# Kernel tuning notes

Hardware: AMD Instinct MI355X
Metric: run time of the kernel (lower is better)

The kernel has to match this reference:

```python
import jax, jax.numpy as jnp
import numpy as np

B, C_IN, T, H, W = 4, 512, 4, 56, 56
G, GP, K = 8, 64, 56            # groups, group_planes, kernel_size (H == K)
OUT = G * GP                     # out_channels = 512
EPS = 1e-5


def setup_inputs() -> dict:
    key = jax.random.key(0)
    ks = jax.random.split(key, 9)
    x = jax.random.normal(ks[0], (B, C_IN, T, H, W), jnp.float32)
    w_qkv = jax.random.normal(ks[1], (2 * OUT, C_IN), jnp.float32) * np.sqrt(1.0 / C_IN)
    g_qkv = jax.random.uniform(ks[2], (2 * OUT,), jnp.float32, 0.5, 1.5)
    b_qkv = jax.random.normal(ks[3], (2 * OUT,), jnp.float32) * 0.1
    relative = jax.random.normal(ks[4], (2 * GP, 2 * K - 1), jnp.float32) * np.sqrt(1.0 / GP)
    g_sim = jax.random.uniform(ks[5], (3 * G,), jnp.float32, 0.5, 1.5)
    b_sim = jax.random.normal(ks[6], (3 * G,), jnp.float32) * 0.1
    g_out = jax.random.uniform(ks[7], (2 * OUT,), jnp.float32, 0.5, 1.5)
    b_out = jax.random.normal(ks[8], (2 * OUT,), jnp.float32) * 0.1
    return {"x": x, "w_qkv": w_qkv, "g_qkv": g_qkv, "b_qkv": b_qkv,
            "relative": relative, "g_sim": g_sim, "b_sim": b_sim,
            "g_out": g_out, "b_out": b_out}


def _bn(x, gamma, beta, axes):
    # training-mode batchnorm: batch stats over `axes`, per channel (dim 1)
    mean = jnp.mean(x, axes, keepdims=True)
    var = jnp.var(x, axes, keepdims=True)
    shp = [1] * x.ndim
    shp[1] = -1
    return gamma.reshape(shp) * (x - mean) * jax.lax.rsqrt(var + EPS) + beta.reshape(shp)


def reference(x, w_qkv, g_qkv, b_qkv, relative, g_sim, b_sim, g_out, b_out):
    # axial='height': (B,C,T,H,W) -> (B,T,W,C,H), attend along H
    xp = jnp.transpose(x, (0, 2, 4, 1, 3)).reshape(B * T * W, C_IN, H)
    # 1x1 Conv1d + BatchNorm1d
    qkv = _bn(jnp.einsum('oc,nch->noh', w_qkv, xp), g_qkv, b_qkv, (0, 2))
    qkv = qkv.reshape(-1, G, 2 * GP, H)
    q, k, v = qkv[:, :, :GP // 2], qkv[:, :, GP // 2:GP], qkv[:, :, GP:]
    qk = jnp.einsum('bgci,bgcj->bgij', q, k)
    # relative position embeddings gathered per (i, j) offset
    idx = jnp.arange(K)[:, None] - jnp.arange(K)[None, :] + K - 1  # (K, K)
    emb = relative[:, idx]                                         # (2*GP, K, K)
    q_e, k_e, v_e = emb[:GP // 2], emb[GP // 2:GP], emb[GP:]
    qr = jnp.einsum('bgci,cij->bgij', q, q_e)
    kr = jnp.swapaxes(jnp.einsum('bgci,cij->bgij', k, k_e), 2, 3)
    sim = _bn(jnp.concatenate([qk, qr, kr], axis=1), g_sim, b_sim, (0, 2, 3))
    sim = sim.reshape(-1, 3, G, H, H).sum(axis=1)
    sim = jax.nn.softmax(sim, axis=3)
    sv = jnp.einsum('bgij,bgcj->bgci', sim, v)
    sve = jnp.einsum('bgij,cij->bgci', sim, v_e)
    out = jnp.concatenate([sv, sve], axis=-1).reshape(-1, 2 * OUT, H)
    out = _bn(out, g_out, b_out, (0, 2))
    out = out.reshape(B, T, W, OUT, 2, H).sum(axis=-2)
    return jnp.transpose(out, (0, 3, 1, 4, 2))  # (B, OUT, T, H, W)
```

## Files before the change

kernel.cpp:

```cpp
#include <hip/hip_runtime.h>
#include <hip/hip_bf16.h>

#define EPS 1e-5f
typedef __hip_bfloat16 bf;
typedef __attribute__((ext_vector_type(8))) short bf16x8;
typedef __attribute__((ext_vector_type(4))) short s16x4;
typedef __attribute__((ext_vector_type(4))) float f32x4;

#define MFMA16(a, b, c) __builtin_amdgcn_mfma_f32_16x16x32_bf16(a, b, c, 0, 0, 0)

#define WS_QSUM     0
#define WS_QSQ      4096
#define WS_SIMSUM   8192
#define WS_SIMSQ    9728
#define WS_OUTSUM   11264
#define WS_OUTSQ    19456
#define WS_ZERO_END 27648
#define WS_AQKV     27648
#define WS_BQKV     28672
#define WS_ASIM     29696
#define WS_BSIM     29728
#define WS_AOUT     29760
#define WS_BOUT     30784

__device__ __forceinline__ void gload_lds16(const void* g, void* l) {
    __builtin_amdgcn_global_load_lds(
        (const __attribute__((address_space(1))) void*)g,
        (__attribute__((address_space(3))) void*)l, 16, 0, 0);
}
__device__ __forceinline__ float bfbits2f(short b) {
    return __uint_as_float(((uint32_t)(unsigned short)b) << 16);
}
__device__ __forceinline__ short f2bfbits(float f) {
    return (short)__hip_bfloat16_raw(__float2bfloat16(f)).x;
}

__global__ __launch_bounds__(256) void k0_transpose(const float* __restrict__ x,
                                                    bf* __restrict__ xbt) {
    int bid = blockIdx.x;
    int h = bid % 56, bt = bid / 56;
    int b = bt >> 2, t = bt & 3;
    __shared__ short tile[512 * 57];
    const float* src = x + (((size_t)(b * 512) * 4 + t) * 3136) + h * 56;
    for (int e = threadIdx.x; e < 512 * 56; e += 256) {
        int c = e / 56, w = e - c * 56;
        tile[c * 57 + w] = f2bfbits(src[(size_t)c * 12544 + w]);
    }
    __syncthreads();
    short* dst = reinterpret_cast<short*>(xbt);
    size_t pbase = ((size_t)bt * 56) * 56 + h;
    for (int e = threadIdx.x; e < 512 * 56; e += 256) {
        int w = e >> 9, c = e & 511;
        dst[(pbase + (size_t)w * 56) * 512 + c] = tile[c * 57 + w];
    }
}

__global__ __launch_bounds__(256) void kw_conv(const float* __restrict__ w, bf* __restrict__ wb) {
    int i = (blockIdx.x * 256 + threadIdx.x) * 4;
#pragma unroll
    for (int u = 0; u < 4; ++u) wb[i + u] = __float2bfloat16(w[i + u]);
}

__global__ __launch_bounds__(256) void kprep(const float* __restrict__ rel,
                                             short* __restrict__ relTq,
                                             short* __restrict__ relTk,
                                             short* __restrict__ relBv) {
    int tid = blockIdx.x * 256 + threadIdx.x;
    if (tid < 3584) {
        int d = tid >> 5, c = tid & 31;
        relTq[tid] = f2bfbits(d < 111 ? rel[c * 111 + d] : 0.f);
        relTk[tid] = f2bfbits(d < 111 ? rel[(32 + c) * 111 + d] : 0.f);
    } else if (tid < 11776) {
        int u = tid - 3584, c = u >> 7, d = u & 127;
        relBv[u] = f2bfbits(d < 111 ? rel[(64 + c) * 111 + d] : 0.f);
    }
}

__global__ __launch_bounds__(256) void k1_mfma(const bf* __restrict__ xbt,
                                               const bf* __restrict__ wb,
                                               short* __restrict__ qkP,
                                               short* __restrict__ vP,
                                               float* __restrict__ qsum,
                                               float* __restrict__ qsq) {
    __shared__ __align__(16) short As[8192];
    __shared__ __align__(16) short Bs[7168];
    int tid = threadIdx.x;
    int g  = blockIdx.x;
    int p0 = blockIdx.y * 112;
    int o0 = g * 128;
    const short* aG = reinterpret_cast<const short*>(wb);
    const short* bG = reinterpret_cast<const short*>(xbt);
    int wv = tid >> 6, l = tid & 63, r16 = l & 15, q4 = l >> 4;

    f32x4 acc[2][7];
#pragma unroll
    for (int i = 0; i < 2; ++i)
#pragma unroll
        for (int j = 0; j < 7; ++j) acc[i][j] = (f32x4){0.f, 0.f, 0.f, 0.f};

    int rowa0 = wv * 32 + r16, rowa1 = rowa0 + 16;

    for (int k0 = 0; k0 < 512; k0 += 64) {
        int ch = tid;
#pragma unroll
        for (int it = 0; it < 4; ++it, ch += 256) {
            int row = ch >> 3, c = ch & 7;
            int gc = (c ^ row) & 7;
            gload_lds16(aG + (((size_t)(o0 + row)) << 9) + k0 + gc * 8, &As[ch << 3]);
        }
        ch = tid;
#pragma unroll
        for (int it = 0; it < 3; ++it, ch += 256) {
            int row = ch >> 3, c = ch & 7;
            int gc = (c ^ row) & 7;
            gload_lds16(bG + (((size_t)(p0 + row)) << 9) + k0 + gc * 8, &Bs[ch << 3]);
        }
        if (tid < 128) {
            int u = tid + 768;
            int row = u >> 3, c = u & 7;
            int gc = (c ^ row) & 7;
            gload_lds16(bG + (((size_t)(p0 + row)) << 9) + k0 + gc * 8, &Bs[u << 3]);
        }
        __syncthreads();
#pragma unroll
        for (int kk = 0; kk < 2; ++kk) {
            int wch = kk * 4 + q4;
            bf16x8 a0 = *reinterpret_cast<const bf16x8*>(&As[rowa0 * 64 + ((wch ^ rowa0) & 7) * 8]);
            bf16x8 a1 = *reinterpret_cast<const bf16x8*>(&As[rowa1 * 64 + ((wch ^ rowa1) & 7) * 8]);
#pragma unroll
            for (int j = 0; j < 7; ++j) {
                int rowb = j * 16 + r16;
                bf16x8 bj = *reinterpret_cast<const bf16x8*>(&Bs[rowb * 64 + ((wch ^ rowb) & 7) * 8]);
                acc[0][j] = MFMA16(a0, bj, acc[0][j]);
                acc[1][j] = MFMA16(a1, bj, acc[1][j]);
            }
        }
        __syncthreads();
    }
    int bkt = blockIdx.y & 3;
#pragma unroll
    for (int i = 0; i < 2; ++i)
#pragma unroll
        for (int r = 0; r < 4; ++r) {
            float sA = 0.f, sB = 0.f;
#pragma unroll
            for (int j = 0; j < 7; ++j) { float v = acc[i][j][r]; sA += v; sB += v * v; }
#pragma unroll
            for (int mk = 1; mk < 16; mk <<= 1) { sA += __shfl_xor(sA, mk); sB += __shfl_xor(sB, mk); }
            if (r16 == 0) {
                int o = o0 + wv * 32 + i * 16 + q4 * 4 + r;
                atomicAdd(&qsum[o * 4 + bkt], sA);
                atomicAdd(&qsq [o * 4 + bkt], sB);
            }
        }
#pragma unroll
    for (int j = 0; j < 7; ++j) {
        int p = p0 + j * 16 + r16;
        size_t rowb = ((size_t)g * 50176 + p) * 64;
#pragma unroll
        for (int i = 0; i < 2; ++i) {
            int op = wv * 32 + i * 16 + q4 * 4;
            s16x4 pk;
#pragma unroll
            for (int r = 0; r < 4; ++r) pk[r] = f2bfbits(acc[i][j][r]);
            short* dst = (op < 64) ? (qkP + rowb + op) : (vP + rowb + (op - 64));
            *reinterpret_cast<s16x4*>(dst) = pk;
        }
    }
}

__global__ __launch_bounds__(256) void k1b_coef(const float* __restrict__ qsum, const float* __restrict__ qsq,
                                                const float* __restrict__ gamma, const float* __restrict__ beta,
                                                float* __restrict__ a_c, float* __restrict__ b_c) {
    int o = blockIdx.x * 256 + threadIdx.x;
    float s = qsum[o * 4] + qsum[o * 4 + 1] + qsum[o * 4 + 2] + qsum[o * 4 + 3];
    float s2 = qsq[o * 4] + qsq[o * 4 + 1] + qsq[o * 4 + 2] + qsq[o * 4 + 3];
    float inv = 1.f / 50176.f;
    float mean = s * inv;
    float var = s2 * inv - mean * mean;
    float a = gamma[o] * rsqrtf(var + EPS);
    a_c[o] = a; b_c[o] = beta[o] - a * mean;
}

__global__ __launch_bounds__(512) void kbn2(const short* __restrict__ qkP,
                                            short* __restrict__ vP,
                                            const float* __restrict__ aq, const float* __restrict__ bq,
                                            const short* __restrict__ relTq,
                                            const short* __restrict__ relTk,
                                            float* __restrict__ ssum, float* __restrict__ ssq) {
    __shared__ __align__(16) short qkTl[5120];
    __shared__ short vtl[64 * 57];
    __shared__ float red[48];
    int blk = blockIdx.x, n = blk >> 3, g = blk & 7, tid = threadIdx.x;
    size_t sb = ((size_t)g * 50176 + (size_t)n * 56) * 64;
    const short* qsrc = qkP + sb;
    short* vsrc = vP + sb;
    for (int u = tid; u < 448; u += 512) {
        int i = u >> 3, c0 = (u & 7) << 3;
        bf16x8 raw = *reinterpret_cast<const bf16x8*>(qsrc + i * 64 + c0);
        bf16x8 t;
#pragma unroll
        for (int uu = 0; uu < 8; ++uu) {
            int o = g * 128 + c0 + uu;
            t[uu] = f2bfbits(aq[o] * bfbits2f(raw[uu]) + bq[o]);
        }
        *reinterpret_cast<bf16x8*>(&qkTl[((c0 & 32) ? 2560 : 0) + i * 40 + (c0 & 31)]) = t;
    }
    for (int u = tid; u < 640; u += 512) {
        int part = u / 320, r = u - part * 320;
        qkTl[part * 2560 + (56 + r / 40) * 40 + (r % 40)] = 0;
    }
    for (int u = tid; u < 448; u += 512) {
        int i = u >> 3, c0 = (u & 7) << 3;
        bf16x8 raw = *reinterpret_cast<const bf16x8*>(vsrc + i * 64 + c0);
#pragma unroll
        for (int uu = 0; uu < 8; ++uu) {
            int o = g * 128 + 64 + c0 + uu;
            vtl[(c0 + uu) * 57 + i] = f2bfbits(aq[o] * bfbits2f(raw[uu]) + bq[o]);
        }
    }
    __syncthreads();
    for (int u = tid; u < 448; u += 512) {
        int c = u / 7, h0 = (u - c * 7) * 8;
        bf16x8 t;
#pragma unroll
        for (int uu = 0; uu < 8; ++uu) t[uu] = vtl[c * 57 + h0 + uu];
        *reinterpret_cast<bf16x8*>(vsrc + c * 56 + h0) = t;
    }
    int w = tid >> 6, l = tid & 63, m = w >> 1, s = w & 1, la = l & 15, lb = l >> 4;
    bf16x8 aqf = *reinterpret_cast<const bf16x8*>(&qkTl[(m * 16 + la) * 40 + lb * 8]);
    bf16x8 akf = *reinterpret_cast<const bf16x8*>(&qkTl[2560 + (m * 16 + la) * 40 + lb * 8]);
    float s0 = 0, s1 = 0, s2v = 0, q0 = 0, q1 = 0, q2 = 0;
#pragma unroll
    for (int t = 0; t < 2; ++t) {
        int nt = 2 * s + t;
        bf16x8 bk = *reinterpret_cast<const bf16x8*>(&qkTl[2560 + (nt * 16 + la) * 40 + lb * 8]);
        f32x4 acc = {0, 0, 0, 0};
        acc = MFMA16(aqf, bk, acc);
        int j = nt * 16 + la;
        if (j < 56) {
#pragma unroll
            for (int r = 0; r < 4; ++r) {
                int i = m * 16 + lb * 4 + r;
                if (i < 56) { float v = acc[r]; s0 += v; q0 += v * v; }
            }
        }
    }
    int ndt = s ? 3 : 4, dt0 = s * 4;
    for (int t = 0; t < ndt; ++t) {
        int dt = dt0 + t;
        bf16x8 br = *reinterpret_cast<const bf16x8*>(relTq + (dt * 16 + la) * 32 + lb * 8);
        f32x4 acc = {0, 0, 0, 0};
        acc = MFMA16(aqf, br, acc);
        int d = dt * 16 + la;
#pragma unroll
        for (int r = 0; r < 4; ++r) {
            int i = m * 16 + lb * 4 + r;
            if (i < 56 && d >= i && d <= i + 55) { float v = acc[r]; s1 += v; q1 += v * v; }
        }
    }
    for (int t = 0; t < ndt; ++t) {
        int dt = dt0 + t;
        bf16x8 br = *reinterpret_cast<const bf16x8*>(relTk + (dt * 16 + la) * 32 + lb * 8);
        f32x4 acc = {0, 0, 0, 0};
        acc = MFMA16(akf, br, acc);
        int d = dt * 16 + la;
#pragma unroll
        for (int r = 0; r < 4; ++r) {
            int j = m * 16 + lb * 4 + r;
            if (j < 56 && d >= j && d <= j + 55) { float v = acc[r]; s2v += v; q2 += v * v; }
        }
    }
    float vals[6] = {s0, s1, s2v, q0, q1, q2};
#pragma unroll
    for (int v = 0; v < 6; ++v) {
        for (int off = 32; off; off >>= 1) vals[v] += __shfl_down(vals[v], off);
        if (l == 0) red[v * 8 + w] = vals[v];
    }
    __syncthreads();
    if (tid < 6) {
        float tot = 0;
#pragma unroll
        for (int k = 0; k < 8; ++k) tot += red[tid * 8 + k];
        int comp = (tid < 3) ? tid : tid - 3;
        int ch = comp * 8 + g;
        int bkt = blk & 63;
        atomicAdd((tid < 3 ? ssum : ssq) + ch * 64 + bkt, tot);
    }
}

__global__ void k2b_coef(const float* __restrict__ ssum, const float* __restrict__ ssq,
                         const float* __restrict__ gs, const float* __restrict__ bs,
                         float* __restrict__ a_c, float* __restrict__ b_c) {
    int c = threadIdx.x;
    if (c >= 24) return;
    float s = 0, s2 = 0;
    for (int k = 0; k < 64; ++k) { s += ssum[c * 64 + k]; s2 += ssq[c * 64 + k]; }
    float inv = 1.f / 2809856.f;
    float mean = s * inv;
    float var = s2 * inv - mean * mean;
    float a = gs[c] * rsqrtf(var + EPS);
    a_c[c] = a; b_c[c] = bs[c] - a * mean;
}

__global__ __launch_bounds__(512, 6) void k3_mfma(const short* __restrict__ relTq,
                                                  const short* __restrict__ relTk,
                                                  const short* __restrict__ relBv,
                                                  short* __restrict__ qkP,
                                                  short* __restrict__ vP,
                                                  const float* __restrict__ aq, const float* __restrict__ bq,
                                                  const float* __restrict__ asim, const float* __restrict__ bsim,
                                                  float* __restrict__ osum, float* __restrict__ osq) {
    __shared__ __align__(16) char smem[51680];
    short* qkTl = (short*)smem;
    float* qkl  = (float*)(smem + 10240);
    short* Sql  = (short*)(smem + 23008);
    short* Krl  = (short*)(smem + 35776);
    short* simB = (short*)(smem + 23008);
    short* Pb   = (short*)(smem + 32224);
    short* vBl  = (short*)smem;
    float* red  = (float*)(smem + 49632);

    int blk = blockIdx.x, n = blk >> 3, g = blk & 7, tid = threadIdx.x;
    size_t sb = ((size_t)g * 50176 + (size_t)n * 56) * 64;
    short* svdst = qkP + sb;
    short* vHs   = vP + sb;
    for (int u = tid; u < 448; u += 512) {
        int i = u >> 3, c0 = (u & 7) << 3;
        bf16x8 raw = *reinterpret_cast<const bf16x8*>(svdst + i * 64 + c0);
        bf16x8 t;
#pragma unroll
        for (int uu = 0; uu < 8; ++uu) {
            int o = g * 128 + c0 + uu;
            t[uu] = f2bfbits(aq[o] * bfbits2f(raw[uu]) + bq[o]);
        }
        *reinterpret_cast<bf16x8*>(&qkTl[((c0 & 32) ? 2560 : 0) + i * 40 + (c0 & 31)]) = t;
    }
    for (int u = tid; u < 640; u += 512) {
        int part = u / 320, r = u - part * 320;
        qkTl[part * 2560 + (56 + r / 40) * 40 + (r % 40)] = 0;
    }
    __syncthreads();

    int w = tid >> 6, l = tid & 63, m = w >> 1, s = w & 1, la = l & 15, lb = l >> 4;
    {
        bf16x8 aqf = *reinterpret_cast<const bf16x8*>(&qkTl[(m * 16 + la) * 40 + lb * 8]);
        bf16x8 akf = *reinterpret_cast<const bf16x8*>(&qkTl[(64 + m * 16 + la) * 40 + lb * 8]);
#pragma unroll
        for (int t = 0; t < 2; ++t) {
            int nt = 2 * s + t;
            bf16x8 bk = *reinterpret_cast<const bf16x8*>(&qkTl[(64 + nt * 16 + la) * 40 + lb * 8]);
            f32x4 acc = {0, 0, 0, 0};
            acc = MFMA16(aqf, bk, acc);
            int j = nt * 16 + la;
            if (j < 56) {
#pragma unroll
                for (int r = 0; r < 4; ++r) {
                    int i = m * 16 + lb * 4 + r;
                    if (i < 56) qkl[i * 57 + j] = acc[r];
                }
            }
        }
        int ndt = s ? 3 : 4, dt0 = s * 4;
        for (int t = 0; t < ndt; ++t) {
            int dt = dt0 + t;
            bf16x8 br = *reinterpret_cast<const bf16x8*>(relTq + (dt * 16 + la) * 32 + lb * 8);
            f32x4 acc = {0, 0, 0, 0};
            acc = MFMA16(aqf, br, acc);
            int d = dt * 16 + la;
#pragma unroll
            for (int r = 0; r < 4; ++r) {
                int i = m * 16 + lb * 4 + r;
                if (i < 56) Sql[i * 114 + d] = f2bfbits(acc[r]);
            }
        }
        for (int t = 0; t < ndt; ++t) {
            int dt = dt0 + t;
            bf16x8 br = *reinterpret_cast<const bf16x8*>(relTk + (dt * 16 + la) * 32 + lb * 8);
            f32x4 acc = {0, 0, 0, 0};
            acc = MFMA16(akf, br, acc);
            int d = dt * 16 + la;
#pragma unroll
            for (int r = 0; r < 4; ++r) {
                int j = m * 16 + lb * 4 + r;
                if (j < 56) Krl[j * 114 + d] = f2bfbits(acc[r]);
            }
        }
    }
    __syncthreads();

    for (int u = tid; u < 448; u += 512) {
        int c = u / 7, ch = u - c * 7;
        bf16x8 raw = *reinterpret_cast<const bf16x8*>(vHs + c * 56 + ch * 8);
        *reinterpret_cast<bf16x8*>(&vBl[c * 72 + ch * 8]) = raw;
    }
    if (tid < 128) {
        int c = tid >> 1, chp = tid & 1;
        bf16x8 z = {0, 0, 0, 0, 0, 0, 0, 0};
        *reinterpret_cast<bf16x8*>(&vBl[c * 72 + 56 + chp * 8]) = z;
    }
    float a0 = asim[g], a1 = asim[8 + g], a2 = asim[16 + g];
    float bb = bsim[g] + bsim[8 + g] + bsim[16 + g];
    float p[7];
#pragma unroll
    for (int rr = 0; rr < 7; ++rr) {
        int i = w * 7 + rr;
        float sc = -1e30f;
        if (l < 56) {
            sc = a0 * qkl[i * 57 + l]
               + a1 * bfbits2f(Sql[i * 114 + (i - l + 55)])
               + a2 * bfbits2f(Krl[l * 114 + (l - i + 55)]) + bb;
        }
        float mx = sc;
#pragma unroll
        for (int off = 32; off; off >>= 1) mx = fmaxf(mx, __shfl_xor(mx, off));
        float e = (l < 56) ? __expf(sc - mx) : 0.f;
        float su = e;
#pragma unroll
        for (int off = 32; off; off >>= 1) su += __shfl_xor(su, off);
        p[rr] = e / su;
    }
    __syncthreads();

#pragma unroll
    for (int rr = 0; rr < 7; ++rr) {
        int i = w * 7 + rr;
        short pv = f2bfbits(p[rr]);
        simB[i * 72 + l] = (l < 56) ? pv : (short)0;
        if (l < 56) Pb[i * 136 + (i - l + 55)] = pv;
        if (l < i || l > i + 55) Pb[i * 136 + l] = 0;
        if (l > i - 9) Pb[i * 136 + l + 64] = 0;
        if (l < 8) Pb[i * 136 + l + 128] = 0;
    }
    __syncthreads();

    f32x4 sva[2]  = {{0, 0, 0, 0}, {0, 0, 0, 0}};
    f32x4 svea[2] = {{0, 0, 0, 0}, {0, 0, 0, 0}};
#pragma unroll
    for (int ks = 0; ks < 2; ++ks) {
        bf16x8 av = *reinterpret_cast<const bf16x8*>(&vBl[(m * 16 + la) * 72 + ks * 32 + lb * 8]);
#pragma unroll
        for (int t = 0; t < 2; ++t) {
            int nt = 2 * s + t;
            bf16x8 bsf = *reinterpret_cast<const bf16x8*>(&simB[(nt * 16 + la) * 72 + ks * 32 + lb * 8]);
            sva[t] = MFMA16(av, bsf, sva[t]);
        }
    }
#pragma unroll
    for (int ks = 0; ks < 4; ++ks) {
        bf16x8 ar = *reinterpret_cast<const bf16x8*>(relBv + (m * 16 + la) * 128 + ks * 32 + lb * 8);
#pragma unroll
        for (int t = 0; t < 2; ++t) {
            int nt = 2 * s + t;
            bf16x8 bp = *reinterpret_cast<const bf16x8*>(&Pb[(nt * 16 + la) * 136 + ks * 32 + lb * 8]);
            svea[t] = MFMA16(ar, bp, svea[t]);
        }
    }
    float st0[4] = {0, 0, 0, 0}, st1[4] = {0, 0, 0, 0}, st2[4] = {0, 0, 0, 0}, st3[4] = {0, 0, 0, 0};
#pragma unroll
    for (int t = 0; t < 2; ++t) {
        int i = (2 * s + t) * 16 + la;
        bool ok = i < 56;
#pragma unroll
        for (int r = 0; r < 4; ++r) {
            int c = m * 16 + lb * 4 + r;
            float va = sva[t][r], ve = svea[t][r];
            if (ok) {
                svdst[c * 56 + i] = f2bfbits(va);
                vHs  [c * 56 + i] = f2bfbits(ve);
                st0[r] += va; st1[r] += va * va; st2[r] += ve; st3[r] += ve * ve;
            }
        }
    }
#pragma unroll
    for (int r = 0; r < 4; ++r) {
#pragma unroll
        for (int mk = 1; mk < 16; mk <<= 1) {
            st0[r] += __shfl_xor(st0[r], mk);
            st1[r] += __shfl_xor(st1[r], mk);
            st2[r] += __shfl_xor(st2[r], mk);
            st3[r] += __shfl_xor(st3[r], mk);
        }
    }
    if (la == 0) {
#pragma unroll
        for (int r = 0; r < 4; ++r) {
            int c = m * 16 + lb * 4 + r;
            red[(0 * 64 + c) * 2 + s] = st0[r];
            red[(1 * 64 + c) * 2 + s] = st1[r];
            red[(2 * 64 + c) * 2 + s] = st2[r];
            red[(3 * 64 + c) * 2 + s] = st3[r];
        }
    }
    __syncthreads();
    if (tid < 64) {
        int c = tid, o2 = (g * 64 + c) * 2, bkt = blk & 7;
        atomicAdd(&osum[o2 * 8 + bkt],       red[(0 * 64 + c) * 2] + red[(0 * 64 + c) * 2 + 1]);
        atomicAdd(&osq [o2 * 8 + bkt],       red[(1 * 64 + c) * 2] + red[(1 * 64 + c) * 2 + 1]);
        atomicAdd(&osum[(o2 + 1) * 8 + bkt], red[(2 * 64 + c) * 2] + red[(2 * 64 + c) * 2 + 1]);
        atomicAdd(&osq [(o2 + 1) * 8 + bkt], red[(3 * 64 + c) * 2] + red[(3 * 64 + c) * 2 + 1]);
    }
}

__global__ __launch_bounds__(256) void k3b_coef(const float* __restrict__ osum, const float* __restrict__ osq,
                                                const float* __restrict__ go, const float* __restrict__ bo,
                                                float* __restrict__ a_c, float* __restrict__ b_c) {
    int o = blockIdx.x * 256 + threadIdx.x;
    float s = 0, s2 = 0;
#pragma unroll
    for (int k = 0; k < 8; ++k) { s += osum[o * 8 + k]; s2 += osq[o * 8 + k]; }
    float inv = 1.f / 50176.f;
    float mean = s * inv;
    float var = s2 * inv - mean * mean;
    float a = go[o] * rsqrtf(var + EPS);
    a_c[o] = a; b_c[o] = bo[o] - a * mean;
}

__global__ __launch_bounds__(256) void k4_out(const short* __restrict__ svq,
                                              const short* __restrict__ sve,
                                              const float* __restrict__ ao, const float* __restrict__ bo,
                                              float* __restrict__ out) {
    int blk = blockIdx.x;
    int oc = blk & 511, bt = blk >> 9;
    int b = bt >> 2, tt = bt & 3;
    int g = oc >> 6, c = oc & 63;
    __shared__ float tile[56][57];
    int tid = threadIdx.x;
    int o_sv = oc * 2, o_sve = oc * 2 + 1;
    float asv = ao[o_sv], bsv = bo[o_sv], asve = ao[o_sve], bsve = bo[o_sve];
    float badd = bsv + bsve;
    int nbase = (b * 4 + tt) * 56;
    for (int e = tid; e < 3136; e += 256) {
        int wq = e / 56, h = e - wq * 56;
        size_t idx = ((size_t)g * 50176 + (size_t)(nbase + wq) * 56) * 64 + c * 56 + h;
        tile[wq][h] = asv * bfbits2f(svq[idx]) + asve * bfbits2f(sve[idx]) + badd;
    }
    __syncthreads();
    size_t ob = ((size_t)(b * 512 + oc) * 4 + tt) * 3136;
    for (int e = tid; e < 3136; e += 256) {
        int h = e / 56, wq = e - h * 56;
        out[ob + h * 56 + wq] = tile[wq][h];
    }
}

extern "C" void kernel_launch(void* const* d_in, const int* in_sizes, int n_in,
                              void* d_out, int out_size, void* d_ws, size_t ws_size,
                              hipStream_t stream) {
    (void)in_sizes; (void)n_in; (void)out_size; (void)ws_size;
    const float* x     = (const float*)d_in[0];
    const float* w_qkv = (const float*)d_in[1];
    const float* g_qkv = (const float*)d_in[2];
    const float* b_qkv = (const float*)d_in[3];
    const float* rel   = (const float*)d_in[4];
    const float* g_sim = (const float*)d_in[5];
    const float* b_sim = (const float*)d_in[6];
    const float* g_out = (const float*)d_in[7];
    const float* b_out = (const float*)d_in[8];
    float* ws  = (float*)d_ws;
    float* out = (float*)d_out;
    short* qkP = (short*)((char*)d_ws + 131072);
    short* vP  = (short*)((char*)d_ws + 51511296);
    bf*    xbt = (bf*)d_out;
    bf*    wb  = (bf*)((char*)d_out + 51380224);
    short* relTq = (short*)((char*)d_out + 73400320);
    short* relTk = relTq + 3584;
    short* relBv = relTk + 3584;

    hipMemsetAsync(ws, 0, WS_ZERO_END * sizeof(float), stream);
    k0_transpose<<<896, 256, 0, stream>>>(x, xbt);
    kw_conv<<<512, 256, 0, stream>>>(w_qkv, wb);
    kprep<<<46, 256, 0, stream>>>(rel, relTq, relTk, relBv);
    k1_mfma<<<dim3(8, 448), 256, 0, stream>>>(xbt, wb, qkP, vP, ws + WS_QSUM, ws + WS_QSQ);
    k1b_coef<<<4, 256, 0, stream>>>(ws + WS_QSUM, ws + WS_QSQ, g_qkv, b_qkv,
                                    ws + WS_AQKV, ws + WS_BQKV);
    kbn2<<<7168, 512, 0, stream>>>(qkP, vP, ws + WS_AQKV, ws + WS_BQKV,
                                   relTq, relTk, ws + WS_SIMSUM, ws + WS_SIMSQ);
    k2b_coef<<<1, 64, 0, stream>>>(ws + WS_SIMSUM, ws + WS_SIMSQ, g_sim, b_sim,
                                   ws + WS_ASIM, ws + WS_BSIM);
    k3_mfma<<<7168, 512, 0, stream>>>(relTq, relTk, relBv, qkP, vP,
                                      ws + WS_AQKV, ws + WS_BQKV,
                                      ws + WS_ASIM, ws + WS_BSIM,
                                      ws + WS_OUTSUM, ws + WS_OUTSQ);
    k3b_coef<<<4, 256, 0, stream>>>(ws + WS_OUTSUM, ws + WS_OUTSQ, g_out, b_out,
                                    ws + WS_AOUT, ws + WS_BOUT);
    k4_out<<<8192, 256, 0, stream>>>(qkP, vP, ws + WS_AOUT, ws + WS_BOUT, out);
}
```

Measured before the change: 466.5 us.

## Transpose Sql/Krl LDS layout for packed stores, prefetch V early, add MFMA priority

Stores the relative-position projections Sql and Krl transposed in LDS (offset-major, stride 60), so each lane writes four packed bf16 values with one 64-bit store instead of four scalar stores. The V tile global load is issued at kernel start into registers and written to LDS after the barrier, hiding its latency behind the first phase. s_setprio is raised around the MFMA sections to favour matrix issue. This adds a little shared memory and register pressure in a kernel launched with 512 threads and a 6-blocks-per-CU bound, which may lower occupancy or cause spills.

```diff
diff --git a/kernel.cpp b/kernel.cpp
--- a/kernel.cpp
+++ b/kernel.cpp
@@ -311,20 +311,26 @@
                                                   const float* __restrict__ aq, const float* __restrict__ bq,
                                                   const float* __restrict__ asim, const float* __restrict__ bsim,
                                                   float* __restrict__ osum, float* __restrict__ osq) {
-    __shared__ __align__(16) char smem[51680];
+    __shared__ __align__(16) char smem[51936];
     short* qkTl = (short*)smem;
     float* qkl  = (float*)(smem + 10240);
     short* Sql  = (short*)(smem + 23008);
-    short* Krl  = (short*)(smem + 35776);
+    short* Krl  = (short*)(smem + 36448);
     short* simB = (short*)(smem + 23008);
     short* Pb   = (short*)(smem + 32224);
     short* vBl  = (short*)smem;
-    float* red  = (float*)(smem + 49632);
+    float* red  = (float*)(smem + 49888);
 
     int blk = blockIdx.x, n = blk >> 3, g = blk & 7, tid = threadIdx.x;
     size_t sb = ((size_t)g * 50176 + (size_t)n * 56) * 64;
     short* svdst = qkP + sb;
     short* vHs   = vP + sb;
+
+    bf16x8 vreg = {0, 0, 0, 0, 0, 0, 0, 0};
+    int vc = tid / 7, vch = tid - vc * 7;
+    if (tid < 448)
+        vreg = *reinterpret_cast<const bf16x8*>(vHs + vc * 56 + vch * 8);
+
     for (int u = tid; u < 448; u += 512) {
         int i = u >> 3, c0 = (u & 7) << 3;
         bf16x8 raw = *reinterpret_cast<const bf16x8*>(svdst + i * 64 + c0);
@@ -343,9 +349,11 @@
     __syncthreads();
 
     int w = tid >> 6, l = tid & 63, m = w >> 1, s = w & 1, la = l & 15, lb = l >> 4;
+    int i0 = m * 16 + lb * 4;
     {
         bf16x8 aqf = *reinterpret_cast<const bf16x8*>(&qkTl[(m * 16 + la) * 40 + lb * 8]);
         bf16x8 akf = *reinterpret_cast<const bf16x8*>(&qkTl[(64 + m * 16 + la) * 40 + lb * 8]);
+        __builtin_amdgcn_s_setprio(1);
 #pragma unroll
         for (int t = 0; t < 2; ++t) {
             int nt = 2 * s + t;
@@ -356,7 +364,7 @@
             if (j < 56) {
 #pragma unroll
                 for (int r = 0; r < 4; ++r) {
-                    int i = m * 16 + lb * 4 + r;
+                    int i = i0 + r;
                     if (i < 56) qkl[i * 57 + j] = acc[r];
                 }
             }
@@ -368,10 +376,11 @@
             f32x4 acc = {0, 0, 0, 0};
             acc = MFMA16(aqf, br, acc);
             int d = dt * 16 + la;
-#pragma unroll
-            for (int r = 0; r < 4; ++r) {
-                int i = m * 16 + lb * 4 + r;
-                if (i < 56) Sql[i * 114 + d] = f2bfbits(acc[r]);
+            if (i0 < 56) {
+                s16x4 pk;
+#pragma unroll
+                for (int r = 0; r < 4; ++r) pk[r] = f2bfbits(acc[r]);
+                *reinterpret_cast<s16x4*>(&Sql[d * 60 + i0]) = pk;
             }
         }
         for (int t = 0; t < ndt; ++t) {
@@ -380,20 +389,19 @@
             f32x4 acc = {0, 0, 0, 0};
             acc = MFMA16(akf, br, acc);
             int d = dt * 16 + la;
-#pragma unroll
-            for (int r = 0; r < 4; ++r) {
-                int j = m * 16 + lb * 4 + r;
-                if (j < 56) Krl[j * 114 + d] = f2bfbits(acc[r]);
-            }
-        }
-    }
-    __syncthreads();
-
-    for (int u = tid; u < 448; u += 512) {
-        int c = u / 7, ch = u - c * 7;
-        bf16x8 raw = *reinterpret_cast<const bf16x8*>(vHs + c * 56 + ch * 8);
-        *reinterpret_cast<bf16x8*>(&vBl[c * 72 + ch * 8]) = raw;
-    }
+            if (i0 < 56) {
+                s16x4 pk;
+#pragma unroll
+                for (int r = 0; r < 4; ++r) pk[r] = f2bfbits(acc[r]);
+                *reinterpret_cast<s16x4*>(&Krl[d * 60 + i0]) = pk;
+            }
+        }
+        __builtin_amdgcn_s_setprio(0);
+    }
+    __syncthreads();
+
+    if (tid < 448)
+        *reinterpret_cast<bf16x8*>(&vBl[vc * 72 + vch * 8]) = vreg;
     if (tid < 128) {
         int c = tid >> 1, chp = tid & 1;
         bf16x8 z = {0, 0, 0, 0, 0, 0, 0, 0};
@@ -408,8 +416,8 @@
         float sc = -1e30f;
         if (l < 56) {
             sc = a0 * qkl[i * 57 + l]
-               + a1 * bfbits2f(Sql[i * 114 + (i - l + 55)])
-               + a2 * bfbits2f(Krl[l * 114 + (l - i + 55)]) + bb;
+               + a1 * bfbits2f(Sql[(i - l + 55) * 60 + i])
+               + a2 * bfbits2f(Krl[(l - i + 55) * 60 + l]) + bb;
         }
         float mx = sc;
 #pragma unroll
@@ -436,6 +444,7 @@
 
     f32x4 sva[2]  = {{0, 0, 0, 0}, {0, 0, 0, 0}};
     f32x4 svea[2] = {{0, 0, 0, 0}, {0, 0, 0, 0}};
+    __builtin_amdgcn_s_setprio(1);
 #pragma unroll
     for (int ks = 0; ks < 2; ++ks) {
         bf16x8 av = *reinterpret_cast<const bf16x8*>(&vBl[(m * 16 + la) * 72 + ks * 32 + lb * 8]);
@@ -456,6 +465,7 @@
             svea[t] = MFMA16(ar, bp, svea[t]);
         }
     }
+    __builtin_amdgcn_s_setprio(0);
     float st0[4] = {0, 0, 0, 0}, st1[4] = {0, 0, 0, 0}, st2[4] = {0, 0, 0, 0}, st3[4] = {0, 0, 0, 0};
 #pragma unroll
     for (int t = 0; t < 2; ++t) {
```

Result: faster. 446.6 us (-4.3%).
